# Performance work log

Hardware: AMD Instinct MI355X
Metric: run time of the kernel (lower is better)

Reference implementation:

```python
import jax, jax.numpy as jnp
import numpy as np

K = 16  # number of neighbors (excluding self)


def setup_inputs() -> dict:
    key = jax.random.key(0)
    k0, k1, k2, k3, k4 = jax.random.split(key, 5)
    B, C, N, Cout = 8, 64, 4096, 64
    x = jax.random.normal(k0, (B, C, N), dtype=jnp.float32)
    s = 1.0 / np.sqrt(C).astype(np.float32)
    W1 = jax.random.normal(k1, (Cout, C), dtype=jnp.float32) * s
    b1 = jax.random.normal(k2, (Cout,), dtype=jnp.float32) * 0.01
    W2 = jax.random.normal(k3, (Cout, C), dtype=jnp.float32) * s
    b2 = jax.random.normal(k4, (Cout,), dtype=jnp.float32) * 0.01
    return {"x": x, "W1": W1, "b1": b1, "W2": W2, "b2": b2}


def _knn_idx(xt):
    # xt: [B, N, C]; squared-euclidean self-KNN, drop self (first / smallest dist)
    sq = jnp.sum(xt * xt, axis=-1)                              # [B, N]
    dist = sq[:, :, None] + sq[:, None, :] - 2.0 * jnp.einsum('bnc,bmc->bnm', xt, xt)
    _, idx = jax.lax.top_k(-dist, K + 1)                        # [B, N, K+1]
    return idx[:, :, 1:]                                        # [B, N, K]


def reference(x, W1, b1, W2, b2):
    # x: [B, C, N]
    xt = jnp.transpose(x, (0, 2, 1))                            # [B, N, C]
    idx = _knn_idx(xt)                                          # [B, N, K]
    # gather neighbors: nb[b,n,k,c] = xt[b, idx[b,n,k], c]
    nb = jax.vmap(lambda xb, ib: xb[ib])(xt, idx)               # [B, N, K, C]
    diff = nb - xt[:, :, None, :]                               # [B, N, K, C]
    message = jnp.einsum('bnkc,oc->bnko', diff, W1) + b1        # conv1 (1x1)
    x_center = jnp.einsum('bnc,oc->bno', xt, W2) + b2           # conv2 (1x1)
    edge = jax.nn.relu(x_center[:, :, None, :] + message)       # [B, N, K, Cout]
    y = jnp.max(edge, axis=2)                                   # [B, N, Cout]
    return jnp.transpose(y, (0, 2, 1))[:, :, None, :]           # [B, Cout, 1, N]
```

## Files before the change

kernel.cpp:

```cpp
#include <hip/hip_runtime.h>
#include <hip/hip_bf16.h>
#include <cstdint>

#define NB    8
#define NPTS  4096
#define NQ    4
#define NT    64
#define PROW  64
#define SENT  0xFF000000u
#define KNN_T 512

typedef __attribute__((ext_vector_type(8))) short bf16x8;
typedef __attribute__((ext_vector_type(4))) float f32x4;

__global__ __launch_bounds__(256) void k_prep(const float* __restrict__ x,
                                              const float* __restrict__ W1,
                                              const float* __restrict__ b1,
                                              const float* __restrict__ W2,
                                              const float* __restrict__ b2,
                                              float* __restrict__ xt,
                                              __hip_bfloat16* __restrict__ xh,
                                              __hip_bfloat16* __restrict__ xl,
                                              float* __restrict__ sq,
                                              float* __restrict__ sqn,
                                              __hip_bfloat16* __restrict__ gh,
                                              __hip_bfloat16* __restrict__ gl,
                                              float* __restrict__ bb) {
  const int t = threadIdx.x;
  if (blockIdx.x == 64) {
    if (blockIdx.y != 0) return;
#pragma unroll 1
    for (int i = t; i < 128 * 64; i += 256) {
      int o = i >> 6, c = i & 63;
      float g = (o < 64) ? W1[o * 64 + c]
                         : (W2[(o - 64) * 64 + c] - W1[(o - 64) * 64 + c]);
      __hip_bfloat16 h = __float2bfloat16(g);
      gh[i] = h;
      gl[i] = __float2bfloat16(g - __bfloat162float(h));
    }
    if (t < 64) bb[t] = b1[t] + b2[t];
    return;
  }
  __shared__ float tile[64][65];
  const int b  = blockIdx.y;
  const int n0 = blockIdx.x * 64;
#pragma unroll
  for (int i = 0; i < 16; ++i) {
    int lin = i * 256 + t;
    int c = lin >> 6, j = lin & 63;
    tile[j][c] = x[(size_t)b * 64 * NPTS + (size_t)c * NPTS + n0 + j];
  }
  __syncthreads();
#pragma unroll
  for (int i = 0; i < 16; ++i) {
    int lin = i * 256 + t;
    int j = lin >> 6, c = lin & 63;
    float v = tile[j][c];
    size_t o = ((size_t)b * NPTS + n0 + j) * 64 + c;
    xt[o] = v;
    __hip_bfloat16 h = __float2bfloat16(v);
    xh[o] = h;
    xl[o] = __float2bfloat16(v - __bfloat162float(h));
  }
  if (t < 64) {
    float s = 0.f;
#pragma unroll
    for (int c = 0; c < 64; ++c) { float v = tile[t][c]; s = fmaf(v, v, s); }
    sq [b * NPTS + t + n0] = s;
    sqn[b * NPTS + t + n0] = fmaf(128.f, s, 32768.f);
  }
}

struct Frag { bf16x8 h0, h1; f32x4 sv; };

__global__ __launch_bounds__(KNN_T, 4) void k_knn(const __hip_bfloat16* __restrict__ xh,
                                                  const float* __restrict__ sqn,
                                                  unsigned* __restrict__ part) {
  __shared__ unsigned bufu[17 * KNN_T];

  const int tid  = threadIdx.x;
  const int w    = tid >> 6;
  const int lane = tid & 63;
  const int quad = lane >> 4, l15 = lane & 15;
  const int rb   = blockIdx.x;
  const int q    = blockIdx.y;
  const int b    = blockIdx.z;
  const size_t xbase = (size_t)b * NPTS * 64;
  const int c0   = q * 1024;
  const int woff = w * 8;
  const int nrow = rb * (KNN_T / 4) + w * 16 + l15;

  const __hip_bfloat16* ph = xh + xbase + (size_t)nrow * 64 + quad * 8;
  bf16x8 rh0 = *(const bf16x8*)(ph);
  bf16x8 rh1 = *(const bf16x8*)(ph + 32);
  rh0 = (rh0 ^ (short)0x8000) + (short)0x0400;
  rh1 = (rh1 ^ (short)0x8000) + (short)0x0400;

  unsigned D[16];
#pragma unroll
  for (int i = 0; i < 16; ++i) D[i] = SENT;
  unsigned thr = SENT | 0xFFFu;
  int cnt = 0;

  auto ldfrag = [&](int t) -> Frag {
    Frag f;
    const __hip_bfloat16* ah = xh + xbase + (size_t)(c0 + t * 16 + l15) * 64 + quad * 8;
    f.h0 = *(const bf16x8*)(ah);
    f.h1 = *(const bf16x8*)(ah + 32);
    f.sv = *(const f32x4*)(sqn + b * NPTS + c0 + t * 16 + quad * 4);
    return f;
  };

  auto flush = [&]() {
    unsigned E[16];
#pragma unroll
    for (int j = 0; j < 16; ++j) E[j] = bufu[j * KNN_T + tid];
#pragma unroll
    for (int j = 0; j < 16; ++j) E[j] = (j < cnt) ? E[j] : 0xFFFFFFFFu;
#pragma unroll
    for (int k = 2; k <= 16; k <<= 1)
#pragma unroll
      for (int j = k >> 1; j > 0; j >>= 1)
#pragma unroll
        for (int i = 0; i < 16; ++i) {
          int l = i ^ j;
          if (l > i) {
            unsigned lo = min(E[i], E[l]), hi = max(E[i], E[l]);
            bool up = ((i & k) == 0);
            E[i] = up ? lo : hi;
            E[l] = up ? hi : lo;
          }
        }
    unsigned T[16];
#pragma unroll
    for (int i = 0; i < 16; ++i) T[i] = min(D[i], E[15 - i]);
#pragma unroll
    for (int j = 8; j > 0; j >>= 1)
#pragma unroll
      for (int i = 0; i < 16; ++i) {
        int l = i ^ j;
        if (l > i) {
          unsigned lo = min(T[i], T[l]);
          T[l] = max(T[i], T[l]);
          T[i] = lo;
        }
      }
#pragma unroll
    for (int i = 0; i < 16; ++i) D[i] = T[i];
    cnt = 0;
    thr = D[15] | 0xFFFu;
  };

  auto ins = [&](float s, int m) {
    unsigned ki  = (unsigned)s;
    unsigned key = (ki << 12) | (unsigned)m;
    bool pass = (key <= thr);
    int slot = pass ? cnt : 16;
    bufu[slot * KNN_T + tid] = key;
    cnt += pass;
  };

  auto compute2 = [&](const Frag& fa, const Frag& fb, int ta, int tb) {
    f32x4 m1 = fa.sv, m3 = fb.sv;
    m1 = __builtin_amdgcn_mfma_f32_16x16x32_bf16(fa.h0, rh0, m1, 0, 0, 0);
    m3 = __builtin_amdgcn_mfma_f32_16x16x32_bf16(fb.h0, rh0, m3, 0, 0, 0);
    m1 = __builtin_amdgcn_mfma_f32_16x16x32_bf16(fa.h1, rh1, m1, 0, 0, 0);
    m3 = __builtin_amdgcn_mfma_f32_16x16x32_bf16(fb.h1, rh1, m3, 0, 0, 0);
    const int ca = c0 + ta * 16 + quad * 4;
    const int cb = c0 + tb * 16 + quad * 4;
#pragma unroll
    for (int i = 0; i < 4; ++i) ins(m1[i], ca + i);
#pragma unroll
    for (int i = 0; i < 4; ++i) ins(m3[i], cb + i);
  };

  Frag a0 = ldfrag(woff), a1 = ldfrag((woff + 1) & 63);
#pragma unroll 1
  for (int it = 0; it < 16; ++it) {
    const int t4 = it * 4;
    const int s2 = (woff + t4 + 2) & 63, s3 = (woff + t4 + 3) & 63;
    Frag b0 = ldfrag(s2), b1 = ldfrag(s3);
    compute2(a0, a1, (woff + t4) & 63, (woff + t4 + 1) & 63);
    if (__any(cnt >= 9)) flush();
    a0 = ldfrag((woff + t4 + 4) & 63);
    a1 = ldfrag((woff + t4 + 5) & 63);
    compute2(b0, b1, s2, s3);
    if (__any(cnt >= 9)) flush();
  }
  flush();

#pragma unroll
  for (int rd = 0; rd < 2; ++rd) {
    const int dx = (rd == 0) ? 16 : 32;
    unsigned Bx[16], T[16];
#pragma unroll
    for (int i = 0; i < 16; ++i) Bx[i] = (unsigned)__shfl_xor((int)D[i], dx);
#pragma unroll
    for (int i = 0; i < 16; ++i) T[i] = min(D[i], Bx[15 - i]);
#pragma unroll
    for (int j = 8; j > 0; j >>= 1)
#pragma unroll
      for (int i = 0; i < 16; ++i) {
        int l = i ^ j;
        if (l > i) {
          unsigned lo = min(T[i], T[l]);
          T[l] = max(T[i], T[l]);
          T[i] = lo;
        }
      }
#pragma unroll
    for (int i = 0; i < 16; ++i) D[i] = T[i];
  }
  if (quad == 0) {
    const size_t base = (size_t)(b * NPTS + nrow) * PROW + (size_t)q * 16;
#pragma unroll
    for (int i = 0; i < 16; ++i) part[base + i] = D[i];
  }
}

__global__ __launch_bounds__(256) void k_mr(const unsigned* __restrict__ part,
                                            const float* __restrict__ xt,
                                            const float* __restrict__ sq,
                                            int* __restrict__ knn) {
  __shared__ unsigned short lc[8][20];
  const int g   = threadIdx.x >> 5;
  const int c   = threadIdx.x & 31;
  const int row = blockIdx.x * 8 + g;
  const uint2 vv = ((const uint2*)(part + (size_t)row * PROW))[c];
  const unsigned v0 = vv.x, v1 = vv.y;
  int r0 = 0, r1 = 0;
#pragma unroll
  for (int j = 0; j < 32; ++j) {
    unsigned a = (unsigned)__shfl((int)v0, j, 32);
    unsigned d = (unsigned)__shfl((int)v1, j, 32);
    r0 += (a < v0) + (d < v0);
    r1 += (a < v1) + (d < v1);
  }
  if (r0 < 20) lc[g][r0] = (unsigned short)(v0 & 0xFFFu);
  if (r1 < 20) lc[g][r1] = (unsigned short)(v1 & 0xFFFu);
  __syncthreads();
  const int b = row >> 12;
  const int m = lc[g][c < 20 ? c : 0];
  const float4* cr = (const float4*)(xt + (size_t)row * 64);
  const float4* mr = (const float4*)(xt + ((size_t)(b << 12) + m) * 64);
  float d = 0.f;
#pragma unroll
  for (int j = 0; j < 16; ++j) {
    float4 a = cr[j], v = mr[j];
    d = fmaf(a.x, v.x, d); d = fmaf(a.y, v.y, d);
    d = fmaf(a.z, v.z, d); d = fmaf(a.w, v.w, d);
  }
  float key = sq[(b << 12) + m] - 2.f * d;
  if (m == (row & 4095)) key = 1e30f;
  int rk = 0;
#pragma unroll
  for (int j = 0; j < 20; ++j) {
    float kj = __shfl(key, j, 32);
    int   mj = __shfl(m, j, 32);
    rk += (kj < key) || ((kj == key) && (mj < m));
  }
  if (c < 20 && rk < 16) knn[(size_t)row * 16 + rk] = m;
}

__global__ __launch_bounds__(256) void k_pq(const __hip_bfloat16* __restrict__ xh,
                                            const __hip_bfloat16* __restrict__ xl,
                                            const __hip_bfloat16* __restrict__ gh,
                                            const __hip_bfloat16* __restrict__ gl,
                                            const float* __restrict__ bb,
                                            float* __restrict__ P,
                                            float* __restrict__ Q) {
  const int tid  = threadIdx.x;
  const int w    = tid >> 6;
  const int lane = tid & 63;
  const int quad = lane >> 4, l15 = lane & 15;
  const int row0 = blockIdx.x * 64 + w * 16;

  const __hip_bfloat16* pa = xh + (size_t)(row0 + l15) * 64 + quad * 8;
  const __hip_bfloat16* pb = xl + (size_t)(row0 + l15) * 64 + quad * 8;
  const bf16x8 ah0 = *(const bf16x8*)(pa);
  const bf16x8 ah1 = *(const bf16x8*)(pa + 32);
  const bf16x8 al0 = *(const bf16x8*)(pb);
  const bf16x8 al1 = *(const bf16x8*)(pb + 32);

#pragma unroll
  for (int ct = 0; ct < 8; ++ct) {
    const __hip_bfloat16* qh = gh + (size_t)(ct * 16 + l15) * 64 + quad * 8;
    const __hip_bfloat16* ql = gl + (size_t)(ct * 16 + l15) * 64 + quad * 8;
    bf16x8 bh0 = *(const bf16x8*)(qh);
    bf16x8 bh1 = *(const bf16x8*)(qh + 32);
    bf16x8 bl0 = *(const bf16x8*)(ql);
    bf16x8 bl1 = *(const bf16x8*)(ql + 32);
    f32x4 m1 = { 0.f, 0.f, 0.f, 0.f };
    f32x4 m2 = m1, m3 = m1, m4 = m1, m5 = m1, m6 = m1;
    m1 = __builtin_amdgcn_mfma_f32_16x16x32_bf16(ah0, bh0, m1, 0, 0, 0);
    m2 = __builtin_amdgcn_mfma_f32_16x16x32_bf16(ah1, bh1, m2, 0, 0, 0);
    m3 = __builtin_amdgcn_mfma_f32_16x16x32_bf16(ah0, bl0, m3, 0, 0, 0);
    m4 = __builtin_amdgcn_mfma_f32_16x16x32_bf16(ah1, bl1, m4, 0, 0, 0);
    m5 = __builtin_amdgcn_mfma_f32_16x16x32_bf16(al0, bh0, m5, 0, 0, 0);
    m6 = __builtin_amdgcn_mfma_f32_16x16x32_bf16(al1, bh1, m6, 0, 0, 0);
    if (ct < 4) {
#pragma unroll
      for (int i = 0; i < 4; ++i) {
        float s = ((m1[i] + m2[i]) + (m3[i] + m4[i])) + (m5[i] + m6[i]);
        P[(size_t)(row0 + quad * 4 + i) * 64 + ct * 16 + l15] = s;
      }
    } else {
      const float bq = bb[(ct - 4) * 16 + l15];
#pragma unroll
      for (int i = 0; i < 4; ++i) {
        float s = ((m1[i] + m2[i]) + (m3[i] + m4[i])) + (m5[i] + m6[i]);
        Q[(size_t)(row0 + quad * 4 + i) * 64 + (ct - 4) * 16 + l15] = s + bq;
      }
    }
  }
}

__global__ __launch_bounds__(512) void k_out(const float* __restrict__ P,
                                             const float* __restrict__ Q,
                                             const int* __restrict__ knn,
                                             float* __restrict__ out) {
  __shared__ float tile[64][65];
  const int b    = blockIdx.y;
  const int n0   = blockIdx.x * 64;
  const int wave = threadIdx.x >> 6;
  const int lane = threadIdx.x & 63;
#pragma unroll 1
  for (int i = 0; i < 8; ++i) {
    const int nl = wave * 8 + i;
    const int gn = b * NPTS + n0 + nl;
    float acc = -1e30f;
    const float qv = Q[(size_t)gn * 64 + lane];
    const int* id = knn + (size_t)gn * 16;
#pragma unroll
    for (int k = 0; k < 16; ++k) {
      int m = id[k];
      float p = P[((size_t)b * NPTS + m) * 64 + lane];
      acc = fmaxf(acc, qv + p);
    }
    tile[nl][lane] = fmaxf(acc, 0.f);
  }
  __syncthreads();
#pragma unroll
  for (int i = 0; i < 8; ++i) {
    const int o = i * 8 + wave;
    out[((size_t)b * 64 + o) * NPTS + n0 + lane] = tile[lane][o];
  }
}

extern "C" void kernel_launch(void* const* d_in, const int* in_sizes, int n_in,
                              void* d_out, int out_size, void* d_ws, size_t ws_size,
                              hipStream_t stream) {
  const float* x  = (const float*)d_in[0];
  const float* W1 = (const float*)d_in[1];
  const float* b1 = (const float*)d_in[2];
  const float* W2 = (const float*)d_in[3];
  const float* b2 = (const float*)d_in[4];
  float* out = (float*)d_out;

  float* ws = (float*)d_ws;
  const size_t NPT_ALL = (size_t)NB * NPTS;
  float*          XT   = ws;
  float*          SQ   = XT + NPT_ALL * 64;
  float*          SQN  = SQ + NPT_ALL;
  __hip_bfloat16* XH   = (__hip_bfloat16*)(SQN + NPT_ALL);
  __hip_bfloat16* XL   = XH + NPT_ALL * 64;
  unsigned*       PART = (unsigned*)(XL + NPT_ALL * 64);
  int*            KNN  = (int*)(PART + NPT_ALL * PROW);
  __hip_bfloat16* GH   = (__hip_bfloat16*)(KNN + NPT_ALL * 16);
  __hip_bfloat16* GL   = GH + 128 * 64;
  float*          BB   = (float*)(GL + 128 * 64);
  float*          Pm   = (float*)PART;
  float*          Qm   = XT;

  k_prep <<<dim3(NPTS / 64 + 1, NB), 256, 0, stream>>>(x, W1, b1, W2, b2,
                                                       XT, XH, XL, SQ, SQN,
                                                       GH, GL, BB);
  k_knn  <<<dim3(NPTS / (KNN_T / 4), NQ, NB), KNN_T, 0, stream>>>(XH, SQN, PART);
  k_mr   <<<dim3(NPT_ALL / 8), 256, 0, stream>>>(PART, XT, SQ, KNN);
  k_pq   <<<dim3(NPT_ALL / 64), 256, 0, stream>>>(XH, XL, GH, GL, BB, Pm, Qm);
  k_out  <<<dim3(NPTS / 64, NB), 512, 0, stream>>>(Pm, Qm, KNN, out);
}
```

Before: 299.1 us.

## Share KNN pruning threshold across quads and split candidate buffer into halves

The running pruning threshold is now the minimum of each lane's 16th-best key across the lanes that hold the same query row (a shuffle-min over the quad groups). This tightens the filter so fewer candidates reach the shared-memory buffer and fewer bitonic flushes run. The single 16-slot candidate buffer is split into two 8-slot halves, one per MFMA output, with separate counters. This shortens the dependency chain on a single counter, but the flush now triggers at a count of 5. Per-wave staggering of the candidate tile order is removed, so all waves walk the tiles in the same order. That may change cache and LDS access patterns.

```diff
diff --git a/kernel.cpp b/kernel.cpp
--- a/kernel.cpp
+++ b/kernel.cpp
@@ -76,7 +76,7 @@
 __global__ __launch_bounds__(KNN_T, 4) void k_knn(const __hip_bfloat16* __restrict__ xh,
                                                   const float* __restrict__ sqn,
                                                   unsigned* __restrict__ part) {
-  __shared__ unsigned bufu[17 * KNN_T];
+  __shared__ unsigned bufu[18 * KNN_T];
 
   const int tid  = threadIdx.x;
   const int w    = tid >> 6;
@@ -87,7 +87,6 @@
   const int b    = blockIdx.z;
   const size_t xbase = (size_t)b * NPTS * 64;
   const int c0   = q * 1024;
-  const int woff = w * 8;
   const int nrow = rb * (KNN_T / 4) + w * 16 + l15;
 
   const __hip_bfloat16* ph = xh + xbase + (size_t)nrow * 64 + quad * 8;
@@ -100,7 +99,7 @@
 #pragma unroll
   for (int i = 0; i < 16; ++i) D[i] = SENT;
   unsigned thr = SENT | 0xFFFu;
-  int cnt = 0;
+  int cntA = 0, cntB = 0;
 
   auto ldfrag = [&](int t) -> Frag {
     Frag f;
@@ -114,9 +113,15 @@
   auto flush = [&]() {
     unsigned E[16];
 #pragma unroll
-    for (int j = 0; j < 16; ++j) E[j] = bufu[j * KNN_T + tid];
-#pragma unroll
-    for (int j = 0; j < 16; ++j) E[j] = (j < cnt) ? E[j] : 0xFFFFFFFFu;
+    for (int j = 0; j < 8; ++j) {
+      E[j]     = bufu[j * KNN_T + tid];
+      E[j + 8] = bufu[(j + 8) * KNN_T + tid];
+    }
+#pragma unroll
+    for (int j = 0; j < 8; ++j) {
+      E[j]     = (j < cntA) ? E[j]     : 0xFFFFFFFFu;
+      E[j + 8] = (j < cntB) ? E[j + 8] : 0xFFFFFFFFu;
+    }
 #pragma unroll
     for (int k = 2; k <= 16; k <<= 1)
 #pragma unroll
@@ -147,45 +152,54 @@
       }
 #pragma unroll
     for (int i = 0; i < 16; ++i) D[i] = T[i];
-    cnt = 0;
-    thr = D[15] | 0xFFFu;
-  };
-
-  auto ins = [&](float s, int m) {
+    cntA = 0; cntB = 0;
+    unsigned t0 = D[15] | 0xFFFu;
+    unsigned t1 = min(t0, (unsigned)__shfl_xor((int)t0, 16));
+    thr = min(t1, (unsigned)__shfl_xor((int)t1, 32));
+  };
+
+  auto insA = [&](float s, int m) {
     unsigned ki  = (unsigned)s;
     unsigned key = (ki << 12) | (unsigned)m;
     bool pass = (key <= thr);
-    int slot = pass ? cnt : 16;
+    int slot = pass ? cntA : 16;
     bufu[slot * KNN_T + tid] = key;
-    cnt += pass;
-  };
-
-  auto compute2 = [&](const Frag& fa, const Frag& fb, int ta, int tb) {
+    cntA += pass;
+  };
+  auto insB = [&](float s, int m) {
+    unsigned ki  = (unsigned)s;
+    unsigned key = (ki << 12) | (unsigned)m;
+    bool pass = (key <= thr);
+    int slot = pass ? cntB + 8 : 17;
+    bufu[slot * KNN_T + tid] = key;
+    cntB += pass;
+  };
+
+  auto compute2 = [&](const Frag& fa, const Frag& fb, int tbase) {
     f32x4 m1 = fa.sv, m3 = fb.sv;
     m1 = __builtin_amdgcn_mfma_f32_16x16x32_bf16(fa.h0, rh0, m1, 0, 0, 0);
     m3 = __builtin_amdgcn_mfma_f32_16x16x32_bf16(fb.h0, rh0, m3, 0, 0, 0);
     m1 = __builtin_amdgcn_mfma_f32_16x16x32_bf16(fa.h1, rh1, m1, 0, 0, 0);
     m3 = __builtin_amdgcn_mfma_f32_16x16x32_bf16(fb.h1, rh1, m3, 0, 0, 0);
-    const int ca = c0 + ta * 16 + quad * 4;
-    const int cb = c0 + tb * 16 + quad * 4;
-#pragma unroll
-    for (int i = 0; i < 4; ++i) ins(m1[i], ca + i);
-#pragma unroll
-    for (int i = 0; i < 4; ++i) ins(m3[i], cb + i);
-  };
-
-  Frag a0 = ldfrag(woff), a1 = ldfrag((woff + 1) & 63);
+    const int cb = c0 + tbase * 16 + quad * 4;
+#pragma unroll
+    for (int i = 0; i < 4; ++i) insA(m1[i], cb + i);
+#pragma unroll
+    for (int i = 0; i < 4; ++i) insB(m3[i], cb + 16 + i);
+  };
+
+  Frag a0 = ldfrag(0), a1 = ldfrag(1);
 #pragma unroll 1
   for (int it = 0; it < 16; ++it) {
     const int t4 = it * 4;
-    const int s2 = (woff + t4 + 2) & 63, s3 = (woff + t4 + 3) & 63;
-    Frag b0 = ldfrag(s2), b1 = ldfrag(s3);
-    compute2(a0, a1, (woff + t4) & 63, (woff + t4 + 1) & 63);
-    if (__any(cnt >= 9)) flush();
-    a0 = ldfrag((woff + t4 + 4) & 63);
-    a1 = ldfrag((woff + t4 + 5) & 63);
-    compute2(b0, b1, s2, s3);
-    if (__any(cnt >= 9)) flush();
+    Frag b0 = ldfrag(t4 + 2), b1 = ldfrag(t4 + 3);
+    compute2(a0, a1, t4);
+    if (__any((cntA | cntB) >= 5)) flush();
+    const int tn = (t4 + 4 < NT) ? t4 + 4 : 62;
+    a0 = ldfrag(tn);
+    a1 = ldfrag(tn + 1);
+    compute2(b0, b1, t4 + 2);
+    if (__any((cntA | cntB) >= 5)) flush();
   }
   flush();
 
```

Measured after the change: 298.2 us. About the same (-0.3%).

## Stage KNN candidate tiles through LDS with async global_load_lds pipeline

Applied to the files above, without the earlier changes.

The KNN kernel drops from 512 to 256 threads per block and now streams candidate tiles into a 4-deep per-wave LDS ring using global_load_lds, with XOR-swizzled addressing and explicit vmcnt waits. Previously each wave loaded fragments straight into registers. The squared-norm bias vector is preloaded into shared memory once, and each wave does one MFMA tile per step instead of two. The flush threshold is now shared across the four quad lanes through shuffles, and the flush trigger is loosened from 9 to 13 buffered entries. These changes aim to hide global load latency and cut register pressure and flush frequency, at the cost of more LDS use, a smaller block and correctness that depends on the hand-written waitcnt placement.

```diff
diff --git a/kernel.cpp b/kernel.cpp
--- a/kernel.cpp
+++ b/kernel.cpp
@@ -8,10 +8,13 @@
 #define NT    64
 #define PROW  64
 #define SENT  0xFF000000u
-#define KNN_T 512
+#define KNN_T 256
 
 typedef __attribute__((ext_vector_type(8))) short bf16x8;
 typedef __attribute__((ext_vector_type(4))) float f32x4;
+
+#define VWAIT(n) do { asm volatile("s_waitcnt vmcnt(" #n ")" ::: "memory"); \
+                      __builtin_amdgcn_sched_barrier(0); } while (0)
 
 __global__ __launch_bounds__(256) void k_prep(const float* __restrict__ x,
                                               const float* __restrict__ W1,
@@ -71,12 +74,12 @@
   }
 }
 
-struct Frag { bf16x8 h0, h1; f32x4 sv; };
-
 __global__ __launch_bounds__(KNN_T, 4) void k_knn(const __hip_bfloat16* __restrict__ xh,
                                                   const float* __restrict__ sqn,
                                                   unsigned* __restrict__ part) {
   __shared__ unsigned bufu[17 * KNN_T];
+  __shared__ float    svb[1024];
+  __shared__ __hip_bfloat16 stg[4][4][1024];
 
   const int tid  = threadIdx.x;
   const int w    = tid >> 6;
@@ -87,8 +90,9 @@
   const int b    = blockIdx.z;
   const size_t xbase = (size_t)b * NPTS * 64;
   const int c0   = q * 1024;
-  const int woff = w * 8;
-  const int nrow = rb * (KNN_T / 4) + w * 16 + l15;
+  const int nrow = rb * 64 + w * 16 + l15;
+
+  *(float4*)&svb[tid * 4] = *(const float4*)(sqn + b * NPTS + c0 + tid * 4);
 
   const __hip_bfloat16* ph = xh + xbase + (size_t)nrow * 64 + quad * 8;
   bf16x8 rh0 = *(const bf16x8*)(ph);
@@ -96,20 +100,29 @@
   rh0 = (rh0 ^ (short)0x8000) + (short)0x0400;
   rh1 = (rh1 ^ (short)0x8000) + (short)0x0400;
 
+  __syncthreads();
+
+  const int rw = lane >> 3, seg = lane & 7;
+  const __hip_bfloat16* g0 = xh + xbase + (size_t)(c0 + rw) * 64 + (seg ^ rw) * 8;
+  const __hip_bfloat16* g1 = g0 + 8 * 64;
+
+  auto stage = [&](int t) {
+    const __hip_bfloat16* s0 = g0 + (size_t)t * (16 * 64);
+    const __hip_bfloat16* s1 = g1 + (size_t)t * (16 * 64);
+    __hip_bfloat16* d = &stg[w][t & 3][0];
+    __builtin_amdgcn_global_load_lds(
+        (const __attribute__((address_space(1))) void*)s0,
+        (__attribute__((address_space(3))) void*)d, 16, 0, 0);
+    __builtin_amdgcn_global_load_lds(
+        (const __attribute__((address_space(1))) void*)s1,
+        (__attribute__((address_space(3))) void*)(d + 512), 16, 0, 0);
+  };
+
   unsigned D[16];
 #pragma unroll
   for (int i = 0; i < 16; ++i) D[i] = SENT;
   unsigned thr = SENT | 0xFFFu;
   int cnt = 0;
-
-  auto ldfrag = [&](int t) -> Frag {
-    Frag f;
-    const __hip_bfloat16* ah = xh + xbase + (size_t)(c0 + t * 16 + l15) * 64 + quad * 8;
-    f.h0 = *(const bf16x8*)(ah);
-    f.h1 = *(const bf16x8*)(ah + 32);
-    f.sv = *(const f32x4*)(sqn + b * NPTS + c0 + t * 16 + quad * 4);
-    return f;
-  };
 
   auto flush = [&]() {
     unsigned E[16];
@@ -148,7 +161,9 @@
 #pragma unroll
     for (int i = 0; i < 16; ++i) D[i] = T[i];
     cnt = 0;
-    thr = D[15] | 0xFFFu;
+    unsigned t0 = D[15] | 0xFFFu;
+    unsigned t1 = min(t0, (unsigned)__shfl_xor((int)t0, 16));
+    thr = min(t1, (unsigned)__shfl_xor((int)t1, 32));
   };
 
   auto ins = [&](float s, int m) {
@@ -160,33 +175,32 @@
     cnt += pass;
   };
 
-  auto compute2 = [&](const Frag& fa, const Frag& fb, int ta, int tb) {
-    f32x4 m1 = fa.sv, m3 = fb.sv;
-    m1 = __builtin_amdgcn_mfma_f32_16x16x32_bf16(fa.h0, rh0, m1, 0, 0, 0);
-    m3 = __builtin_amdgcn_mfma_f32_16x16x32_bf16(fb.h0, rh0, m3, 0, 0, 0);
-    m1 = __builtin_amdgcn_mfma_f32_16x16x32_bf16(fa.h1, rh1, m1, 0, 0, 0);
-    m3 = __builtin_amdgcn_mfma_f32_16x16x32_bf16(fb.h1, rh1, m3, 0, 0, 0);
-    const int ca = c0 + ta * 16 + quad * 4;
-    const int cb = c0 + tb * 16 + quad * 4;
-#pragma unroll
-    for (int i = 0; i < 4; ++i) ins(m1[i], ca + i);
-#pragma unroll
-    for (int i = 0; i < 4; ++i) ins(m3[i], cb + i);
+  const int o0 = l15 * 128 + ((quad ^ (l15 & 7)) << 4);
+  const int o1 = l15 * 128 + (((4 ^ quad) ^ (l15 & 7)) << 4);
+
+  auto consume = [&](int t) {
+    const char* tb = (const char*)&stg[w][t & 3][0];
+    const bf16x8 h0 = *(const bf16x8*)(tb + o0);
+    const bf16x8 h1 = *(const bf16x8*)(tb + o1);
+    f32x4 m = *(const f32x4*)&svb[t * 16 + quad * 4];
+    m = __builtin_amdgcn_mfma_f32_16x16x32_bf16(h0, rh0, m, 0, 0, 0);
+    m = __builtin_amdgcn_mfma_f32_16x16x32_bf16(h1, rh1, m, 0, 0, 0);
+    const int cb = c0 + t * 16 + quad * 4;
+#pragma unroll
+    for (int i = 0; i < 4; ++i) ins(m[i], cb + i);
   };
 
-  Frag a0 = ldfrag(woff), a1 = ldfrag((woff + 1) & 63);
+  stage(0); stage(1); stage(2);
 #pragma unroll 1
-  for (int it = 0; it < 16; ++it) {
-    const int t4 = it * 4;
-    const int s2 = (woff + t4 + 2) & 63, s3 = (woff + t4 + 3) & 63;
-    Frag b0 = ldfrag(s2), b1 = ldfrag(s3);
-    compute2(a0, a1, (woff + t4) & 63, (woff + t4 + 1) & 63);
-    if (__any(cnt >= 9)) flush();
-    a0 = ldfrag((woff + t4 + 4) & 63);
-    a1 = ldfrag((woff + t4 + 5) & 63);
-    compute2(b0, b1, s2, s3);
-    if (__any(cnt >= 9)) flush();
-  }
+  for (int t = 0; t < NT - 3; ++t) {
+    VWAIT(4);
+    stage(t + 3);
+    consume(t);
+    if (__any(cnt >= 13)) flush();
+  }
+  VWAIT(4); consume(NT - 3); if (__any(cnt >= 13)) flush();
+  VWAIT(2); consume(NT - 2); if (__any(cnt >= 13)) flush();
+  VWAIT(0); consume(NT - 1);
   flush();
 
 #pragma unroll
@@ -375,7 +389,7 @@
   k_prep <<<dim3(NPTS / 64 + 1, NB), 256, 0, stream>>>(x, W1, b1, W2, b2,
                                                        XT, XH, XL, SQ, SQN,
                                                        GH, GL, BB);
-  k_knn  <<<dim3(NPTS / (KNN_T / 4), NQ, NB), KNN_T, 0, stream>>>(XH, SQN, PART);
+  k_knn  <<<dim3(NPTS / 64, NQ, NB), KNN_T, 0, stream>>>(XH, SQN, PART);
   k_mr   <<<dim3(NPT_ALL / 8), 256, 0, stream>>>(PART, XT, SQ, KNN);
   k_pq   <<<dim3(NPT_ALL / 64), 256, 0, stream>>>(XH, XL, GH, GL, BB, Pm, Qm);
   k_out  <<<dim3(NPTS / 64, NB), 512, 0, stream>>>(Pm, Qm, KNN, out);
```

Measured after the change: 302.6 us. About the same (+1.2%).

## Restructure KNN: 2 column splits, shared row-norm staging, quad-shared pruning threshold

Applied to the files above, without the earlier changes.

The KNN kernel now splits candidate columns into 2 chunks of 2048 instead of 4 of 1024. Each 256-thread block handles 64 query rows. Candidate norms are staged once into shared memory instead of being read from global memory per fragment. The flush threshold is now the minimum across the four quads sharing a row, which prunes more insertions. This halves the partial-candidate list per row that the merge kernel ranks (32 instead of 64), in exchange for longer per-block loops and fewer blocks.

```diff
diff --git a/kernel.cpp b/kernel.cpp
--- a/kernel.cpp
+++ b/kernel.cpp
@@ -4,11 +4,11 @@
 
 #define NB    8
 #define NPTS  4096
-#define NQ    4
-#define NT    64
-#define PROW  64
+#define NQ    2
+#define NT    128
+#define PROW  32
 #define SENT  0xFF000000u
-#define KNN_T 512
+#define KNN_T 256
 
 typedef __attribute__((ext_vector_type(8))) short bf16x8;
 typedef __attribute__((ext_vector_type(4))) float f32x4;
@@ -77,6 +77,7 @@
                                                   const float* __restrict__ sqn,
                                                   unsigned* __restrict__ part) {
   __shared__ unsigned bufu[17 * KNN_T];
+  __shared__ float    svb[2048];
 
   const int tid  = threadIdx.x;
   const int w    = tid >> 6;
@@ -86,9 +87,14 @@
   const int q    = blockIdx.y;
   const int b    = blockIdx.z;
   const size_t xbase = (size_t)b * NPTS * 64;
-  const int c0   = q * 1024;
-  const int woff = w * 8;
-  const int nrow = rb * (KNN_T / 4) + w * 16 + l15;
+  const int c0   = q * 2048;
+  const int nrow = rb * 64 + w * 16 + l15;
+
+  {
+    const float4* src = (const float4*)(sqn + b * NPTS + c0);
+    ((float4*)svb)[tid]       = src[tid];
+    ((float4*)svb)[tid + 256] = src[tid + 256];
+  }
 
   const __hip_bfloat16* ph = xh + xbase + (size_t)nrow * 64 + quad * 8;
   bf16x8 rh0 = *(const bf16x8*)(ph);
@@ -96,6 +102,8 @@
   rh0 = (rh0 ^ (short)0x8000) + (short)0x0400;
   rh1 = (rh1 ^ (short)0x8000) + (short)0x0400;
 
+  __syncthreads();
+
   unsigned D[16];
 #pragma unroll
   for (int i = 0; i < 16; ++i) D[i] = SENT;
@@ -107,7 +115,7 @@
     const __hip_bfloat16* ah = xh + xbase + (size_t)(c0 + t * 16 + l15) * 64 + quad * 8;
     f.h0 = *(const bf16x8*)(ah);
     f.h1 = *(const bf16x8*)(ah + 32);
-    f.sv = *(const f32x4*)(sqn + b * NPTS + c0 + t * 16 + quad * 4);
+    f.sv = *(const f32x4*)&svb[t * 16 + quad * 4];
     return f;
   };
 
@@ -148,7 +156,9 @@
 #pragma unroll
     for (int i = 0; i < 16; ++i) D[i] = T[i];
     cnt = 0;
-    thr = D[15] | 0xFFFu;
+    unsigned t0 = D[15] | 0xFFFu;
+    unsigned t1 = min(t0, (unsigned)__shfl_xor((int)t0, 16));
+    thr = min(t1, (unsigned)__shfl_xor((int)t1, 32));
   };
 
   auto ins = [&](float s, int m) {
@@ -160,31 +170,30 @@
     cnt += pass;
   };
 
-  auto compute2 = [&](const Frag& fa, const Frag& fb, int ta, int tb) {
+  auto compute2 = [&](const Frag& fa, const Frag& fb, int tbase) {
     f32x4 m1 = fa.sv, m3 = fb.sv;
     m1 = __builtin_amdgcn_mfma_f32_16x16x32_bf16(fa.h0, rh0, m1, 0, 0, 0);
     m3 = __builtin_amdgcn_mfma_f32_16x16x32_bf16(fb.h0, rh0, m3, 0, 0, 0);
     m1 = __builtin_amdgcn_mfma_f32_16x16x32_bf16(fa.h1, rh1, m1, 0, 0, 0);
     m3 = __builtin_amdgcn_mfma_f32_16x16x32_bf16(fb.h1, rh1, m3, 0, 0, 0);
-    const int ca = c0 + ta * 16 + quad * 4;
-    const int cb = c0 + tb * 16 + quad * 4;
+    const int ca = c0 + tbase * 16 + quad * 4;
 #pragma unroll
     for (int i = 0; i < 4; ++i) ins(m1[i], ca + i);
 #pragma unroll
-    for (int i = 0; i < 4; ++i) ins(m3[i], cb + i);
+    for (int i = 0; i < 4; ++i) ins(m3[i], ca + 16 + i);
   };
 
-  Frag a0 = ldfrag(woff), a1 = ldfrag((woff + 1) & 63);
+  Frag a0 = ldfrag(0), a1 = ldfrag(1);
 #pragma unroll 1
-  for (int it = 0; it < 16; ++it) {
+  for (int it = 0; it < NT / 4; ++it) {
     const int t4 = it * 4;
-    const int s2 = (woff + t4 + 2) & 63, s3 = (woff + t4 + 3) & 63;
-    Frag b0 = ldfrag(s2), b1 = ldfrag(s3);
-    compute2(a0, a1, (woff + t4) & 63, (woff + t4 + 1) & 63);
+    Frag b0 = ldfrag(t4 + 2), b1 = ldfrag(t4 + 3);
+    compute2(a0, a1, t4);
     if (__any(cnt >= 9)) flush();
-    a0 = ldfrag((woff + t4 + 4) & 63);
-    a1 = ldfrag((woff + t4 + 5) & 63);
-    compute2(b0, b1, s2, s3);
+    const int tn = (t4 + 4 < NT) ? t4 + 4 : NT - 2;
+    a0 = ldfrag(tn);
+    a1 = ldfrag(tn + 1);
+    compute2(b0, b1, t4 + 2);
     if (__any(cnt >= 9)) flush();
   }
   flush();
@@ -226,18 +235,14 @@
   const int g   = threadIdx.x >> 5;
   const int c   = threadIdx.x & 31;
   const int row = blockIdx.x * 8 + g;
-  const uint2 vv = ((const uint2*)(part + (size_t)row * PROW))[c];
-  const unsigned v0 = vv.x, v1 = vv.y;
-  int r0 = 0, r1 = 0;
+  const unsigned v = part[(size_t)row * PROW + c];
+  int r = 0;
 #pragma unroll
   for (int j = 0; j < 32; ++j) {
-    unsigned a = (unsigned)__shfl((int)v0, j, 32);
-    unsigned d = (unsigned)__shfl((int)v1, j, 32);
-    r0 += (a < v0) + (d < v0);
-    r1 += (a < v1) + (d < v1);
-  }
-  if (r0 < 20) lc[g][r0] = (unsigned short)(v0 & 0xFFFu);
-  if (r1 < 20) lc[g][r1] = (unsigned short)(v1 & 0xFFFu);
+    unsigned a = (unsigned)__shfl((int)v, j, 32);
+    r += (a < v);
+  }
+  if (r < 20) lc[g][r] = (unsigned short)(v & 0xFFFu);
   __syncthreads();
   const int b = row >> 12;
   const int m = lc[g][c < 20 ? c : 0];
@@ -246,9 +251,9 @@
   float d = 0.f;
 #pragma unroll
   for (int j = 0; j < 16; ++j) {
-    float4 a = cr[j], v = mr[j];
-    d = fmaf(a.x, v.x, d); d = fmaf(a.y, v.y, d);
-    d = fmaf(a.z, v.z, d); d = fmaf(a.w, v.w, d);
+    float4 a = cr[j], vv = mr[j];
+    d = fmaf(a.x, vv.x, d); d = fmaf(a.y, vv.y, d);
+    d = fmaf(a.z, vv.z, d); d = fmaf(a.w, vv.w, d);
   }
   float key = sq[(b << 12) + m] - 2.f * d;
   if (m == (row & 4095)) key = 1e30f;
@@ -365,7 +370,7 @@
   __hip_bfloat16* XH   = (__hip_bfloat16*)(SQN + NPT_ALL);
   __hip_bfloat16* XL   = XH + NPT_ALL * 64;
   unsigned*       PART = (unsigned*)(XL + NPT_ALL * 64);
-  int*            KNN  = (int*)(PART + NPT_ALL * PROW);
+  int*            KNN  = (int*)(PART + NPT_ALL * 64);
   __hip_bfloat16* GH   = (__hip_bfloat16*)(KNN + NPT_ALL * 16);
   __hip_bfloat16* GL   = GH + 128 * 64;
   float*          BB   = (float*)(GL + 128 * 64);
@@ -375,7 +380,7 @@
   k_prep <<<dim3(NPTS / 64 + 1, NB), 256, 0, stream>>>(x, W1, b1, W2, b2,
                                                        XT, XH, XL, SQ, SQN,
                                                        GH, GL, BB);
-  k_knn  <<<dim3(NPTS / (KNN_T / 4), NQ, NB), KNN_T, 0, stream>>>(XH, SQN, PART);
+  k_knn  <<<dim3(NPTS / 64, NQ, NB), KNN_T, 0, stream>>>(XH, SQN, PART);
   k_mr   <<<dim3(NPT_ALL / 8), 256, 0, stream>>>(PART, XT, SQ, KNN);
   k_pq   <<<dim3(NPT_ALL / 64), 256, 0, stream>>>(XH, XL, GH, GL, BB, Pm, Qm);
   k_out  <<<dim3(NPTS / 64, NB), 512, 0, stream>>>(Pm, Qm, KNN, out);
```

Result: faster. 274.3 us (-8.3%).
